# Kernel tuning notes

Hardware: AMD Instinct MI355X
Metric: run time of the kernel (lower is better)

The kernel has to match this reference:

```python
import jax, jax.numpy as jnp
import numpy as np

N = 50000      # drug nodes
E = 600000     # edges (avg degree 12)
D = 128        # emb_dim
HOPS = 2       # n_hops
NEFF = 1000    # n_effects
Q = 200000     # number of (node, effect) query pairs


def setup_inputs() -> dict:
    key = jax.random.key(0)
    ks = jax.random.split(key, 9)
    graph_x = jax.random.normal(ks[0], (N, D), dtype=jnp.float32)
    edge_index = jax.random.randint(ks[1], (2, E), 0, N)
    chemical_similarity = jax.random.uniform(ks[2], (E,), dtype=jnp.float32)
    x_nodes = jax.random.randint(ks[3], (Q,), 0, N)
    effect_ids = jax.random.randint(ks[4], (Q,), 0, NEFF)
    # per-hop SAGEConv params: self transform, neighbor transform, bias
    W_self = jax.random.normal(ks[5], (HOPS, D, D), dtype=jnp.float32) / np.sqrt(D)
    W_neigh = jax.random.normal(ks[6], (HOPS, D, D), dtype=jnp.float32) / np.sqrt(D)
    bias = jnp.zeros((HOPS, D), dtype=jnp.float32)
    # xavier-uniform effect embedding table
    lim = np.sqrt(6.0 / (NEFF + D))
    effect_emb = jax.random.uniform(ks[7], (NEFF, D), dtype=jnp.float32, minval=-lim, maxval=lim)
    return {
        "graph_x": graph_x,
        "edge_index": edge_index,
        "x_nodes": x_nodes,
        "effect_ids": effect_ids,
        "chemical_similarity": chemical_similarity,
        "W_self": W_self,
        "W_neigh": W_neigh,
        "bias": bias,
        "effect_emb": effect_emb,
    }


def reference(graph_x, edge_index, x_nodes, effect_ids, chemical_similarity,
              W_self, W_neigh, bias, effect_emb):
    src, dst = edge_index[0], edge_index[1]
    w = chemical_similarity  # [E]
    x = graph_x              # [N, D]
    for h in range(HOPS):
        # weighted-mean neighbor aggregation (SAGEConv with edge weights)
        msg = x[src] * w[:, None]                                  # [E, D]
        agg = jax.ops.segment_sum(msg, dst, num_segments=N)        # [N, D]
        denom = jax.ops.segment_sum(w, dst, num_segments=N)        # [N]
        agg = agg / jnp.maximum(denom, 1e-12)[:, None]
        x = jax.nn.relu(x @ W_self[h] + agg @ W_neigh[h] + bias[h])
    # final gather + effect embedding add
    return x[x_nodes] + effect_emb[effect_ids]                     # [Q, D]
```

## Files before the change

### kernel.cpp

```cpp
#include <hip/hip_runtime.h>
#include <hip/hip_bf16.h>

#define D 128
#define CAP 64
#define BM 64
#define CSTR 32

using bf16x8 = __attribute__((ext_vector_type(8))) short;
using f32x4  = __attribute__((ext_vector_type(4))) float;

static __device__ __forceinline__ unsigned short f2bf(float f) {
    unsigned u = __float_as_uint(f);
    u += 0x7FFF + ((u >> 16) & 1);
    return (unsigned short)(u >> 16);
}
static __device__ __forceinline__ float bf2f(unsigned short s) {
    return __uint_as_float(((unsigned)s) << 16);
}
static __device__ __forceinline__ void acc8(float* a, uint4 v, float w) {
    a[0] += w * bf2f((ushort)(v.x & 0xffff));
    a[1] += w * bf2f((ushort)(v.x >> 16));
    a[2] += w * bf2f((ushort)(v.y & 0xffff));
    a[3] += w * bf2f((ushort)(v.y >> 16));
    a[4] += w * bf2f((ushort)(v.z & 0xffff));
    a[5] += w * bf2f((ushort)(v.z >> 16));
    a[6] += w * bf2f((ushort)(v.w & 0xffff));
    a[7] += w * bf2f((ushort)(v.w >> 16));
}

__global__ __launch_bounds__(256) void prep_fused(
    const float* __restrict__ xin, ushort* __restrict__ xb,
    const float* __restrict__ Ws, const float* __restrict__ Wn,
    ushort* __restrict__ Wt, int* __restrict__ cnt,
    long n8, int wtot, int nzero4, int nConv, int nWt)
{
    const int b = blockIdx.x;
    if (b < nConv) {
        long i = (long)b * 256 + threadIdx.x;
        if (i >= n8) return;
        const float4* p = (const float4*)xin + i * 2;
        float4 a = p[0], v = p[1];
        uint4 o;
        o.x = (unsigned)f2bf(a.x) | ((unsigned)f2bf(a.y) << 16);
        o.y = (unsigned)f2bf(a.z) | ((unsigned)f2bf(a.w) << 16);
        o.z = (unsigned)f2bf(v.x) | ((unsigned)f2bf(v.y) << 16);
        o.w = (unsigned)f2bf(v.z) | ((unsigned)f2bf(v.w) << 16);
        ((uint4*)xb)[i] = o;
    } else if (b < nConv + nWt) {
        int idx = (b - nConv) * 256 + threadIdx.x;
        if (idx >= wtot) return;
        int h   = idx >> 15;
        int rem = idx & 32767;
        int n   = rem >> 8;
        int k   = rem & 255;
        float v = (k < D) ? Ws[(size_t)h * D * D + (size_t)k * D + n]
                          : Wn[(size_t)h * D * D + (size_t)(k - D) * D + n];
        Wt[idx] = f2bf(v);
    } else {
        int idx = (b - nConv - nWt) * 256 + threadIdx.x;
        if (idx >= nzero4) return;
        int4 z = {0, 0, 0, 0};
        ((int4*)cnt)[idx] = z;
    }
}

__global__ __launch_bounds__(256) void fill_edges(
    const int* __restrict__ ei, const float* __restrict__ w,
    int* __restrict__ cnt, int2* __restrict__ pad, int E)
{
    int e = blockIdx.x * 256 + threadIdx.x;
    if (e >= E) return;
    int s = ei[e];
    int d = ei[E + e];
    float wv = w[e];
    int pos = atomicAdd(&cnt[(size_t)d * CSTR], 1);
    if (pos < CAP) {
        pad[(size_t)d * CAP + pos] = make_int2(s, __float_as_int(wv));
    }
}

__global__ __launch_bounds__(256) void aggregate(
    const ushort* __restrict__ x, const int* __restrict__ cnt,
    const int2* __restrict__ pad, ushort* __restrict__ agg, int N)
{
    const int wave = threadIdx.x >> 6;
    const int lane = threadIdx.x & 63;
    const int n = blockIdx.x * 4 + wave;
    if (n >= N) return;
    const int c  = lane & 15;
    const int jj = lane >> 4;

    int deg = cnt[(size_t)n * CSTR];
    if (deg > CAP) deg = CAP;
    const size_t base = (size_t)n * CAP;

    float a[8] = {0.f, 0.f, 0.f, 0.f, 0.f, 0.f, 0.f, 0.f};
    float wsum = 0.f;

    for (int t = 0; t < deg; t += 16) {
        const int j = t + jj * 4;
        int4 p01 = *(const int4*)(pad + base + j);
        int4 p23 = *(const int4*)(pad + base + j + 2);
        const int s0 = (j + 0 < deg) ? p01.x : 0;
        const int s1 = (j + 1 < deg) ? p01.z : 0;
        const int s2 = (j + 2 < deg) ? p23.x : 0;
        const int s3 = (j + 3 < deg) ? p23.z : 0;
        const float w0 = (j + 0 < deg) ? __int_as_float(p01.y) : 0.f;
        const float w1 = (j + 1 < deg) ? __int_as_float(p01.w) : 0.f;
        const float w2 = (j + 2 < deg) ? __int_as_float(p23.y) : 0.f;
        const float w3 = (j + 3 < deg) ? __int_as_float(p23.w) : 0.f;
        uint4 v0 = *(const uint4*)(x + (size_t)s0 * D + c * 8);
        uint4 v1 = *(const uint4*)(x + (size_t)s1 * D + c * 8);
        uint4 v2 = *(const uint4*)(x + (size_t)s2 * D + c * 8);
        uint4 v3 = *(const uint4*)(x + (size_t)s3 * D + c * 8);
        acc8(a, v0, w0);
        acc8(a, v1, w1);
        acc8(a, v2, w2);
        acc8(a, v3, w3);
        wsum += w0 + w1 + w2 + w3;
    }

    #pragma unroll
    for (int i = 0; i < 8; ++i) {
        a[i] += __shfl_xor(a[i], 16, 64);
        a[i] += __shfl_xor(a[i], 32, 64);
    }
    wsum += __shfl_xor(wsum, 16, 64);
    wsum += __shfl_xor(wsum, 32, 64);

    if (jj == 0) {
        const float inv = 1.f / fmaxf(wsum, 1e-12f);
        uint4 o;
        o.x = (unsigned)f2bf(a[0] * inv) | ((unsigned)f2bf(a[1] * inv) << 16);
        o.y = (unsigned)f2bf(a[2] * inv) | ((unsigned)f2bf(a[3] * inv) << 16);
        o.z = (unsigned)f2bf(a[4] * inv) | ((unsigned)f2bf(a[5] * inv) << 16);
        o.w = (unsigned)f2bf(a[6] * inv) | ((unsigned)f2bf(a[7] * inv) << 16);
        *(uint4*)(agg + (size_t)n * D + c * 8) = o;
    }
}

__global__ __launch_bounds__(256) void gemm_mfma(
    const ushort* __restrict__ xin, const ushort* __restrict__ agg,
    const ushort* __restrict__ Wt, const float* __restrict__ bias,
    ushort* __restrict__ xout, int nrows)
{
    __shared__ ushort As[BM][72];
    __shared__ ushort Bs[D][72];
    const int tid  = threadIdx.x;
    const int w    = tid >> 6;
    const int lane = tid & 63;
    const int r16  = lane & 15;
    const int kq   = lane >> 4;
    const int row0 = blockIdx.x * BM;

    f32x4 acc[8];
    #pragma unroll
    for (int nf = 0; nf < 8; ++nf) acc[nf] = {0.f, 0.f, 0.f, 0.f};

    for (int kc = 0; kc < 4; ++kc) {
        {
            const ushort* src = (kc < 2) ? xin : agg;
            const int kb = (kc & 1) * 64;
            const int r = tid >> 2, q = tid & 3;
            const int grow = row0 + r;
            if (grow < nrows) {
                const uint4* gp = (const uint4*)(src + (size_t)grow * D + kb + q * 16);
                uint4 v0 = gp[0], v1 = gp[1];
                *(uint4*)&As[r][q * 16]     = v0;
                *(uint4*)&As[r][q * 16 + 8] = v1;
            } else {
                uint4 z = {0u, 0u, 0u, 0u};
                *(uint4*)&As[r][q * 16]     = z;
                *(uint4*)&As[r][q * 16 + 8] = z;
            }
        }
        {
            const int n = tid >> 1, h2 = tid & 1;
            const uint4* gp = (const uint4*)(Wt + (size_t)n * 256 + kc * 64 + h2 * 32);
            uint4 v0 = gp[0], v1 = gp[1], v2 = gp[2], v3 = gp[3];
            *(uint4*)&Bs[n][h2 * 32]      = v0;
            *(uint4*)&Bs[n][h2 * 32 + 8]  = v1;
            *(uint4*)&Bs[n][h2 * 32 + 16] = v2;
            *(uint4*)&Bs[n][h2 * 32 + 24] = v3;
        }
        __syncthreads();
        #pragma unroll
        for (int kk = 0; kk < 64; kk += 32) {
            bf16x8 a = *(const bf16x8*)&As[w * 16 + r16][kk + kq * 8];
            #pragma unroll
            for (int nf = 0; nf < 8; ++nf) {
                bf16x8 b = *(const bf16x8*)&Bs[nf * 16 + r16][kk + kq * 8];
                acc[nf] = __builtin_amdgcn_mfma_f32_16x16x32_bf16(a, b, acc[nf], 0, 0, 0);
            }
        }
        __syncthreads();
    }
    #pragma unroll
    for (int nf = 0; nf < 8; ++nf) {
        const int col = nf * 16 + r16;
        const float bv = bias[col];
        #pragma unroll
        for (int i = 0; i < 4; ++i) {
            const int grow = row0 + w * 16 + kq * 4 + i;
            if (grow < nrows) {
                float v = fmaxf(acc[nf][i] + bv, 0.f);
                xout[(size_t)grow * D + col] = f2bf(v);
            }
        }
    }
}

__global__ __launch_bounds__(256) void out_kernel(
    const ushort* __restrict__ x, const float* __restrict__ emb,
    const int* __restrict__ xn, const int* __restrict__ eid,
    float* __restrict__ out, int Q)
{
    long g = (long)blockIdx.x * 256 + threadIdx.x;
    long tot = (long)Q * 32;
    if (g >= tot) return;
    int q = (int)(g >> 5);
    int c = (int)(g & 31);
    int nq = xn[q], ef = eid[q];
    ushort4 xv = *((const ushort4*)(x + (size_t)nq * D) + c);
    float4  ev = *((const float4*)(emb + (size_t)ef * D) + c);
    float4 o = {bf2f(xv.x) + ev.x, bf2f(xv.y) + ev.y,
                bf2f(xv.z) + ev.z, bf2f(xv.w) + ev.w};
    ((float4*)out)[g] = o;
}

extern "C" void kernel_launch(void* const* d_in, const int* in_sizes, int n_in,
                              void* d_out, int out_size, void* d_ws, size_t ws_size,
                              hipStream_t stream)
{
    const float* graph_x   = (const float*)d_in[0];
    const int*   edge_idx  = (const int*)d_in[1];
    const int*   x_nodes   = (const int*)d_in[2];
    const int*   effect_id = (const int*)d_in[3];
    const float* chem      = (const float*)d_in[4];
    const float* W_self    = (const float*)d_in[5];
    const float* W_neigh   = (const float*)d_in[6];
    const float* bias      = (const float*)d_in[7];
    const float* eff_emb   = (const float*)d_in[8];

    const int N    = in_sizes[0] / D;
    const int E    = in_sizes[4];
    const int Q    = in_sizes[2];
    const int HOPS = in_sizes[7] / D;

    char* wsp = (char*)d_ws;
    int*    cnt  = (int*)wsp;     wsp += (size_t)N * CSTR * 4;
    int2*   pad  = (int2*)wsp;    wsp += (size_t)N * CAP * 8;
    ushort* xb   = (ushort*)wsp;  wsp += (size_t)N * D * 2;
    ushort* aggb = (ushort*)wsp;  wsp += (size_t)N * D * 2;
    ushort* x1b  = (ushort*)wsp;  wsp += (size_t)N * D * 2;
    ushort* Wt   = (ushort*)wsp;  wsp += (size_t)HOPS * D * 256 * 2;

    const long n8     = (long)N * D / 8;
    const int  wtot   = HOPS * D * 256;
    const int  nzero4 = N * CSTR / 4;
    const int  nConv  = (int)((n8 + 255) / 256);
    const int  nWt    = (wtot + 255) / 256;
    const int  nZero  = (nzero4 + 255) / 256;
    prep_fused<<<nConv + nWt + nZero, 256, 0, stream>>>(
        graph_x, xb, W_self, W_neigh, Wt, cnt, n8, wtot, nzero4, nConv, nWt);

    fill_edges<<<(E + 255) / 256, 256, 0, stream>>>(
        edge_idx, chem, cnt, pad, E);

    const int aggGrid  = (N + 3) / 4;
    const int gemmGrid = (N + BM - 1) / BM;

    for (int h = 0; h < HOPS; ++h) {
        const ushort* xin = (h == 0) ? xb : x1b;
        aggregate<<<aggGrid, 256, 0, stream>>>(xin, cnt, pad, aggb, N);
        gemm_mfma<<<gemmGrid, 256, 0, stream>>>(
            xin, aggb, Wt + (size_t)h * D * 256, bias + (size_t)h * D, x1b, N);
    }

    long tot = (long)Q * 32;
    out_kernel<<<(int)((tot + 255) / 256), 256, 0, stream>>>(
        x1b, eff_emb, x_nodes, effect_id, (float*)d_out, Q);
}
```

Measured before the change: 143.4 us.

## Split per-node edge buckets into four sub-buckets to spread atomic contention

Each destination node's padded adjacency list becomes four 16-slot sub-buckets with their own padded counters, chosen by edge index modulo four. This spreads atomic contention across separate cache lines in fill_edges. In aggregate, each 16-lane group now walks its own sub-bucket instead of interleaving over one list. The zeroed counter array doubles in size, and each sub-bucket holds at most 16 edges, so a node whose edges pile into one sub-bucket can drop edges the old 64-slot cap would have kept.

Result: slower. 154.7 us (+7.8%).

```diff
diff --git a/kernel.cpp b/kernel.cpp
--- a/kernel.cpp
+++ b/kernel.cpp
@@ -4,7 +4,8 @@
 #define D 128
 #define CAP 64
 #define BM 64
-#define CSTR 32
+#define NSUB 4
+#define SUBSTR 16
 
 using bf16x8 = __attribute__((ext_vector_type(8))) short;
 using f32x4  = __attribute__((ext_vector_type(4))) float;
@@ -73,9 +74,10 @@
     int s = ei[e];
     int d = ei[E + e];
     float wv = w[e];
-    int pos = atomicAdd(&cnt[(size_t)d * CSTR], 1);
-    if (pos < CAP) {
-        pad[(size_t)d * CAP + pos] = make_int2(s, __float_as_int(wv));
+    const int sub = e & (NSUB - 1);
+    int pos = atomicAdd(&cnt[((size_t)d * NSUB + sub) * SUBSTR], 1);
+    if (pos < 16) {
+        pad[(size_t)d * CAP + sub * 16 + pos] = make_int2(s, __float_as_int(wv));
     }
 }
 
@@ -90,25 +92,24 @@
     const int c  = lane & 15;
     const int jj = lane >> 4;
 
-    int deg = cnt[(size_t)n * CSTR];
-    if (deg > CAP) deg = CAP;
-    const size_t base = (size_t)n * CAP;
+    int dj = cnt[((size_t)n * NSUB + jj) * SUBSTR];
+    if (dj > 16) dj = 16;
+    const size_t base = (size_t)n * CAP + jj * 16;
 
     float a[8] = {0.f, 0.f, 0.f, 0.f, 0.f, 0.f, 0.f, 0.f};
     float wsum = 0.f;
 
-    for (int t = 0; t < deg; t += 16) {
-        const int j = t + jj * 4;
-        int4 p01 = *(const int4*)(pad + base + j);
-        int4 p23 = *(const int4*)(pad + base + j + 2);
-        const int s0 = (j + 0 < deg) ? p01.x : 0;
-        const int s1 = (j + 1 < deg) ? p01.z : 0;
-        const int s2 = (j + 2 < deg) ? p23.x : 0;
-        const int s3 = (j + 3 < deg) ? p23.z : 0;
-        const float w0 = (j + 0 < deg) ? __int_as_float(p01.y) : 0.f;
-        const float w1 = (j + 1 < deg) ? __int_as_float(p01.w) : 0.f;
-        const float w2 = (j + 2 < deg) ? __int_as_float(p23.y) : 0.f;
-        const float w3 = (j + 3 < deg) ? __int_as_float(p23.w) : 0.f;
+    for (int t = 0; t < dj; t += 4) {
+        int4 p01 = *(const int4*)(pad + base + t);
+        int4 p23 = *(const int4*)(pad + base + t + 2);
+        const int s0 = (t + 0 < dj) ? p01.x : 0;
+        const int s1 = (t + 1 < dj) ? p01.z : 0;
+        const int s2 = (t + 2 < dj) ? p23.x : 0;
+        const int s3 = (t + 3 < dj) ? p23.z : 0;
+        const float w0 = (t + 0 < dj) ? __int_as_float(p01.y) : 0.f;
+        const float w1 = (t + 1 < dj) ? __int_as_float(p01.w) : 0.f;
+        const float w2 = (t + 2 < dj) ? __int_as_float(p23.y) : 0.f;
+        const float w3 = (t + 3 < dj) ? __int_as_float(p23.w) : 0.f;
         uint4 v0 = *(const uint4*)(x + (size_t)s0 * D + c * 8);
         uint4 v1 = *(const uint4*)(x + (size_t)s1 * D + c * 8);
         uint4 v2 = *(const uint4*)(x + (size_t)s2 * D + c * 8);
@@ -248,7 +249,7 @@
     const int HOPS = in_sizes[7] / D;
 
     char* wsp = (char*)d_ws;
-    int*    cnt  = (int*)wsp;     wsp += (size_t)N * CSTR * 4;
+    int*    cnt  = (int*)wsp;     wsp += (size_t)N * NSUB * SUBSTR * 4;
     int2*   pad  = (int2*)wsp;    wsp += (size_t)N * CAP * 8;
     ushort* xb   = (ushort*)wsp;  wsp += (size_t)N * D * 2;
     ushort* aggb = (ushort*)wsp;  wsp += (size_t)N * D * 2;
@@ -257,7 +258,7 @@
 
     const long n8     = (long)N * D / 8;
     const int  wtot   = HOPS * D * 256;
-    const int  nzero4 = N * CSTR / 4;
+    const int  nzero4 = N * NSUB * SUBSTR / 4;
     const int  nConv  = (int)((n8 + 255) / 256);
     const int  nWt    = (wtot + 255) / 256;
     const int  nZero  = (nzero4 + 255) / 256;
```
